# Kernel optimization log

Measured on AMD Instinct MI355X. Metric: run time of the kernel, lower is better.

The kernel has to match this reference:

```python
import jax, jax.numpy as jnp
import numpy as np

LAM = 5.0
NUM_STEPS = 100
B, N, D = 16, 1024, 256


def l2_normalize(x, eps=1e-12):
    # tf.math.l2_normalize: x * rsqrt(max(sum(x^2), eps))
    sq = jnp.sum(x * x, axis=-1, keepdims=True)
    return x * jax.lax.rsqrt(jnp.maximum(sq, eps))


def normalize_pij(P):
    return P / jnp.sum(P, axis=(1, 2), keepdims=True)


def sinkhorn_step(P):
    # a_vec = b_vec = ones(N), so u = 1/col_sum, v = 1/row_sum
    P = P / jnp.sum(P, axis=2, keepdims=True)   # scale rows
    P = P / jnp.sum(P, axis=1, keepdims=True)   # scale cols
    return P


def setup_inputs() -> dict:
    key = jax.random.key(0)
    kA, kB = jax.random.split(key)
    fA = jax.random.normal(kA, (B, N, D), dtype=jnp.float32)
    fB = jax.random.normal(kB, (B, N, D), dtype=jnp.float32)
    return {"fA": fA, "fB": fB}


def reference(fA, fB):
    fA = l2_normalize(fA)
    fB = l2_normalize(fB)
    Sij = jnp.einsum("bnd,bmd->bnm", fA, fB)          # [B, N, N]
    Cij = jnp.clip(-Sij, -15.0 / LAM, 15.0 / LAM)

    # batch_compute_optimal_transport
    P = jnp.exp(-LAM * Cij)
    P = normalize_pij(P)

    def step(P, _):
        return sinkhorn_step(P), None

    P, _ = jax.lax.scan(step, P, None, length=NUM_STEPS)

    # straight-through style re-parameterization
    alpha_beta = jax.lax.stop_gradient(P * jnp.exp(LAM * Cij))
    P0 = alpha_beta * jnp.exp(-LAM * Cij)
    P0 = normalize_pij(P0)
    P_out = sinkhorn_step(P0)
    return (P_out, Sij)
```

## Files before the change

kernel.cpp:

```cpp
#include <hip/hip_runtime.h>
#include <stdint.h>

#define NB 16
#define NN 1024
#define ND 256

typedef __bf16 bf16x8 __attribute__((ext_vector_type(8)));
typedef float f32x4 __attribute__((ext_vector_type(4)));

__device__ __forceinline__ unsigned short f2bf(float x){
  unsigned u = __builtin_bit_cast(unsigned, x);
  u += 0x7FFFu + ((u >> 16) & 1u);
  return (unsigned short)(u >> 16);
}
__device__ __forceinline__ float bflo(unsigned u){ return __builtin_bit_cast(float, u << 16); }
__device__ __forceinline__ float bfhi(unsigned u){ return __builtin_bit_cast(float, u & 0xFFFF0000u); }

__global__ __launch_bounds__(256) void norm_cast_kernel(
    const float* __restrict__ fA, const float* __restrict__ fB,
    unsigned short* __restrict__ Abf, unsigned short* __restrict__ Bbf)
{
  int task = blockIdx.x * 4 + (threadIdx.x >> 6);
  int lane = threadIdx.x & 63;
  const float* src = (task < NB*NN) ? fA : fB;
  unsigned short* dst = (task < NB*NN) ? Abf : Bbf;
  int row = (task < NB*NN) ? task : task - NB*NN;
  float4 x = ((const float4*)(src + (size_t)row*ND))[lane];
  float sq = x.x*x.x + x.y*x.y + x.z*x.z + x.w*x.w;
  #pragma unroll
  for (int off = 32; off > 0; off >>= 1) sq += __shfl_xor(sq, off);
  float s = rsqrtf(fmaxf(sq, 1e-12f));
  ushort4 o;
  o.x = f2bf(x.x*s); o.y = f2bf(x.y*s); o.z = f2bf(x.z*s); o.w = f2bf(x.w*s);
  ((ushort4*)(dst + (size_t)row*ND))[lane] = o;
}

#define LDK 40

__global__ __launch_bounds__(256) void gemm_exp_kernel(
    const unsigned short* __restrict__ Abf, const unsigned short* __restrict__ Bbf,
    float* __restrict__ S, unsigned short* __restrict__ Kg)
{
  __shared__ __align__(16) unsigned short As[128*LDK];
  __shared__ __align__(16) unsigned short Bs[128*LDK];
  const int b = blockIdx.z;
  const int mbase = blockIdx.y * 128;
  const int nbase = blockIdx.x * 128;
  const int t = threadIdx.x;
  const int lane = t & 63;
  const int wave = t >> 6;
  const int wm = wave >> 1, wn = wave & 1;
  const int quad = lane >> 4, l16 = lane & 15;

  const unsigned short* Ab = Abf + (size_t)b*NN*ND;
  const unsigned short* Bb = Bbf + (size_t)b*NN*ND;

  f32x4 acc[4][4];
  #pragma unroll
  for (int i=0;i<4;i++)
    #pragma unroll
    for (int j=0;j<4;j++) acc[i][j] = (f32x4){0.f,0.f,0.f,0.f};

  for (int k0 = 0; k0 < ND; k0 += 32){
    __syncthreads();
    #pragma unroll
    for (int i=0;i<2;i++){
      int chunk = t + 256*i;
      int row = chunk >> 2, seg = chunk & 3;
      *(uint4*)(&As[row*LDK + seg*8]) = *(const uint4*)(Ab + (size_t)(mbase+row)*ND + k0 + seg*8);
      *(uint4*)(&Bs[row*LDK + seg*8]) = *(const uint4*)(Bb + (size_t)(nbase+row)*ND + k0 + seg*8);
    }
    __syncthreads();
    bf16x8 af[4], bg[4];
    #pragma unroll
    for (int i=0;i<4;i++){
      af[i] = *(const bf16x8*)(&As[(wm*64 + i*16 + l16)*LDK + quad*8]);
      bg[i] = *(const bf16x8*)(&Bs[(wn*64 + i*16 + l16)*LDK + quad*8]);
    }
    #pragma unroll
    for (int i=0;i<4;i++)
      #pragma unroll
      for (int j=0;j<4;j++)
        acc[i][j] = __builtin_amdgcn_mfma_f32_16x16x32_bf16(af[i], bg[j], acc[i][j], 0, 0, 0);
  }

  float* Sb = S + (size_t)b*NN*NN;
  unsigned short* Kb = Kg + (size_t)b*NN*NN;
  #pragma unroll
  for (int i=0;i<4;i++){
    #pragma unroll
    for (int j=0;j<4;j++){
      int n = nbase + wn*64 + j*16 + l16;
      #pragma unroll
      for (int v=0;v<4;v++){
        int m = mbase + wm*64 + i*16 + quad*4 + v;
        float sv = acc[i][j][v];
        Sb[(size_t)m*NN + n] = sv;
        float sc = fminf(fmaxf(sv, -3.f), 3.f);
        Kb[(size_t)m*NN + n] = f2bf(__expf(5.f*sc));
      }
    }
  }
}

__global__ __launch_bounds__(1024) void sinkhorn_kernel(
    const unsigned short* __restrict__ Kg, float* __restrict__ P,
    float* __restrict__ slots)
{
  __shared__ __align__(16) float v[NN];
  __shared__ __align__(16) float part[NN];
  __shared__ __align__(16) float u[64];

  const int blk = blockIdx.x;
  const int b  = blk & 15;
  const int rb = blk >> 4;
  const int t = threadIdx.x;
  const int w = t >> 6;
  const int l = t & 63;

  const unsigned short* Kgb = Kg + ((size_t)(b*NN + rb*64))*NN;

  unsigned kcol[32];
  #pragma unroll
  for (int k=0;k<32;k++){
    unsigned lo = Kgb[(size_t)(2*k)*NN + t];
    unsigned hi = Kgb[(size_t)(2*k+1)*NN + t];
    kcol[k] = lo | (hi << 16);
  }
  unsigned krow[32];
  {
    const uint4* rs = (const uint4*)(Kgb + (size_t)l*NN + w*64);
    #pragma unroll
    for (int k=0;k<8;k++){
      uint4 q4 = rs[k];
      krow[4*k+0]=q4.x; krow[4*k+1]=q4.y; krow[4*k+2]=q4.z; krow[4*k+3]=q4.w;
    }
  }
  v[t] = 1.0f;
  __syncthreads();

  const float4* v4 = (const float4*)v;
  const float4* u4 = (const float4*)u;
  float* sl_b = slots + (size_t)b*3*16*NN;
  float* my_slot = sl_b + (size_t)rb*NN + t;

  int buf = 0;
  float vt = 1.0f;
  for (int it = 0; it < 101; it++){
    float rsum = 0.f;
    #pragma unroll
    for (int k=0;k<16;k++){
      float4 vv = v4[w*16 + k];
      unsigned ka = krow[2*k], kb = krow[2*k+1];
      rsum += bflo(ka)*vv.x + bfhi(ka)*vv.y + bflo(kb)*vv.z + bfhi(kb)*vv.w;
    }
    part[w*64 + l] = rsum;
    __syncthreads();
    if (t < 64){
      float s = 0.f;
      #pragma unroll
      for (int q=0;q<16;q++) s += part[q*64 + t];
      u[t] = 1.0f / s;
    }
    __syncthreads();
    float csum = 0.f;
    #pragma unroll
    for (int k=0;k<16;k++){
      float4 uu = u4[k];
      unsigned ka = kcol[2*k], kb = kcol[2*k+1];
      csum += bflo(ka)*uu.x + bfhi(ka)*uu.y + bflo(kb)*uu.z + bfhi(kb)*uu.w;
    }
    __hip_atomic_store(my_slot + (size_t)buf*16*NN, csum,
                       __ATOMIC_RELAXED, __HIP_MEMORY_SCOPE_AGENT);
    const float* base = sl_b + (size_t)buf*16*NN + t;
    float cs;
    for (;;){
      float s0 = 0.f; bool ok = true;
      #pragma unroll
      for (int p=0;p<16;p++){
        float x = __hip_atomic_load(base + (size_t)p*NN,
                                    __ATOMIC_RELAXED, __HIP_MEMORY_SCOPE_AGENT);
        ok &= (x != 0.f);
        s0 += x;
      }
      if (ok){ cs = s0; break; }
      __builtin_amdgcn_s_sleep(1);
    }
    int prev = (buf == 0) ? 2 : buf - 1;
    __hip_atomic_store(my_slot + (size_t)prev*16*NN, 0.f,
                       __ATOMIC_RELAXED, __HIP_MEMORY_SCOPE_AGENT);
    vt = 1.0f / cs;
    v[t] = vt;
    buf = (buf == 2) ? 0 : buf + 1;
    __syncthreads();
  }

  float* Pb = P + ((size_t)(b*NN + rb*64))*NN;
  #pragma unroll
  for (int k=0;k<16;k++){
    float4 uu = u4[k];
    unsigned ka = kcol[2*k], kb = kcol[2*k+1];
    Pb[(size_t)(4*k+0)*NN + t] = bflo(ka)*uu.x*vt;
    Pb[(size_t)(4*k+1)*NN + t] = bfhi(ka)*uu.y*vt;
    Pb[(size_t)(4*k+2)*NN + t] = bflo(kb)*uu.z*vt;
    Pb[(size_t)(4*k+3)*NN + t] = bfhi(kb)*uu.w*vt;
  }
}

extern "C" void kernel_launch(void* const* d_in, const int* in_sizes, int n_in,
                              void* d_out, int out_size, void* d_ws, size_t ws_size,
                              hipStream_t stream)
{
  const float* fA = (const float*)d_in[0];
  const float* fB = (const float*)d_in[1];
  float* Pout = (float*)d_out;
  float* Sout = Pout + (size_t)NB*NN*NN;
  unsigned short* Kg = (unsigned short*)d_out;

  unsigned short* Abf = (unsigned short*)d_ws;
  unsigned short* Bbf = Abf + (size_t)NB*NN*ND;
  float* slots = (float*)((char*)d_ws + (size_t)16*1024*1024);

  hipMemsetAsync(slots, 0, (size_t)NB*3*16*NN*4, stream);
  norm_cast_kernel<<<dim3(8192), dim3(256), 0, stream>>>(fA, fB, Abf, Bbf);
  gemm_exp_kernel<<<dim3(8,8,NB), dim3(256), 0, stream>>>(Abf, Bbf, Sout, Kg);
  sinkhorn_kernel<<<dim3(256), dim3(1024), 0, stream>>>(Kg, Pout, slots);
}
```

Baseline: 1.742 ms.

## Probe for L2-coherent fast path and use workgroup-scope polling in Sinkhorn exchange

Adds a startup handshake in which the 16 blocks of each batch check whether stores and loads at workgroup scope (sc0 only) are seen by the other blocks within a deadline, then agree on a per-batch verdict. If every block passes, the per-iteration cross-block column-sum exchange uses workgroup-scope stores and inline-asm batched sc0 loads instead of agent-scope atomics. The aim is lower latency for the 101 inter-block barrier rounds. The cost is a startup probe, and correctness now depends on the blocks of a batch sharing a coherent L2/XCD, with a fallback to the old path otherwise.

Result: slower. 3.842 ms (+120.6%).

```diff
diff --git a/kernel.cpp b/kernel.cpp
--- a/kernel.cpp
+++ b/kernel.cpp
@@ -103,13 +103,56 @@
   }
 }
 
+__device__ __forceinline__ void store_l2(float* p, float x){
+  __hip_atomic_store(p, x, __ATOMIC_RELAXED, __HIP_MEMORY_SCOPE_WORKGROUP);
+}
+
+__device__ __forceinline__ bool poll8(const float* base, unsigned voff, float thr, float& sum){
+  float x0,x1,x2,x3,x4,x5,x6,x7; unsigned a;
+  asm volatile(
+    "v_mov_b32 %8, %9\n\t"
+    "global_load_dword %0, %8, %10 sc0\n\t"
+    "v_add_u32 %8, 0x1000, %8\n\t"
+    "global_load_dword %1, %8, %10 sc0\n\t"
+    "v_add_u32 %8, 0x1000, %8\n\t"
+    "global_load_dword %2, %8, %10 sc0\n\t"
+    "v_add_u32 %8, 0x1000, %8\n\t"
+    "global_load_dword %3, %8, %10 sc0\n\t"
+    "v_add_u32 %8, 0x1000, %8\n\t"
+    "global_load_dword %4, %8, %10 sc0\n\t"
+    "v_add_u32 %8, 0x1000, %8\n\t"
+    "global_load_dword %5, %8, %10 sc0\n\t"
+    "v_add_u32 %8, 0x1000, %8\n\t"
+    "global_load_dword %6, %8, %10 sc0\n\t"
+    "v_add_u32 %8, 0x1000, %8\n\t"
+    "global_load_dword %7, %8, %10 sc0\n\t"
+    "s_waitcnt vmcnt(0)"
+    : "=&v"(x0),"=&v"(x1),"=&v"(x2),"=&v"(x3),
+      "=&v"(x4),"=&v"(x5),"=&v"(x6),"=&v"(x7),"=&v"(a)
+    : "v"(voff), "s"((uint64_t)(uintptr_t)base)
+    : "memory");
+  bool ok = (x0>thr)&(x1>thr)&(x2>thr)&(x3>thr)&(x4>thr)&(x5>thr)&(x6>thr)&(x7>thr);
+  sum = ((x0+x1)+(x2+x3))+((x4+x5)+(x6+x7));
+  return ok;
+}
+
+__device__ __forceinline__ bool poll16(const float* base, int t, float thr, float& sum){
+  float s0, s1;
+  bool o0 = poll8(base, (unsigned)(t*4), thr, s0);
+  bool o1 = poll8(base, (unsigned)(t*4) + 8u*4096u, thr, s1);
+  sum = s0 + s1;
+  return o0 & o1;
+}
+
 __global__ __launch_bounds__(1024) void sinkhorn_kernel(
     const unsigned short* __restrict__ Kg, float* __restrict__ P,
-    float* __restrict__ slots)
+    float* __restrict__ slots, unsigned* __restrict__ verdict)
 {
   __shared__ __align__(16) float v[NN];
   __shared__ __align__(16) float part[NN];
   __shared__ __align__(16) float u[64];
+  __shared__ int bad;
+  __shared__ int fastflag;
 
   const int blk = blockIdx.x;
   const int b  = blk & 15;
@@ -137,11 +180,57 @@
     }
   }
   v[t] = 1.0f;
-  __syncthreads();
+
+  float* sl_b = slots + (size_t)b*4*16*NN;
+  float* probe_base = sl_b + (size_t)3*16*NN;
+  {
+    float dum;
+    store_l2(probe_base + (size_t)rb*NN + t, 1.0f);
+    bool ok = false;
+    unsigned long long dl = __builtin_amdgcn_s_memrealtime() + 100000ull;
+    for(;;){
+      ok = poll16(probe_base, t, 0.5f, dum);
+      if (ok) break;
+      if (__builtin_amdgcn_s_memrealtime() > dl) break;
+      __builtin_amdgcn_s_sleep(1);
+    }
+    if (ok){
+      store_l2(probe_base + (size_t)rb*NN + t, 2.0f);
+      dl = __builtin_amdgcn_s_memrealtime() + 100000ull;
+      for(;;){
+        if (poll16(probe_base, t, 1.5f, dum)) break;
+        if (__builtin_amdgcn_s_memrealtime() > dl){ ok = false; break; }
+        __builtin_amdgcn_s_sleep(1);
+      }
+    }
+    if (t == 0) bad = 0;
+    __syncthreads();
+    if (!ok) bad = 1;
+    __syncthreads();
+    if (t == 0){
+      unsigned my = bad ? 2u : 1u;
+      __hip_atomic_store(&verdict[b*16 + rb], my,
+                         __ATOMIC_RELAXED, __HIP_MEMORY_SCOPE_AGENT);
+      int f = 1;
+      for(;;){
+        bool pending = false; f = 1;
+        for (int p=0;p<16;p++){
+          unsigned x = __hip_atomic_load(&verdict[b*16 + p],
+                                         __ATOMIC_RELAXED, __HIP_MEMORY_SCOPE_AGENT);
+          if (x == 0u){ pending = true; break; }
+          if (x != 1u) f = 0;
+        }
+        if (!pending) break;
+        __builtin_amdgcn_s_sleep(8);
+      }
+      fastflag = f;
+    }
+    __syncthreads();
+  }
+  const bool fastf = (fastflag != 0);
 
   const float4* v4 = (const float4*)v;
   const float4* u4 = (const float4*)u;
-  float* sl_b = slots + (size_t)b*3*16*NN;
   float* my_slot = sl_b + (size_t)rb*NN + t;
 
   int buf = 0;
@@ -170,25 +259,35 @@
       unsigned ka = kcol[2*k], kb = kcol[2*k+1];
       csum += bflo(ka)*uu.x + bfhi(ka)*uu.y + bflo(kb)*uu.z + bfhi(kb)*uu.w;
     }
-    __hip_atomic_store(my_slot + (size_t)buf*16*NN, csum,
-                       __ATOMIC_RELAXED, __HIP_MEMORY_SCOPE_AGENT);
-    const float* base = sl_b + (size_t)buf*16*NN + t;
     float cs;
-    for (;;){
-      float s0 = 0.f; bool ok = true;
-      #pragma unroll
-      for (int p=0;p<16;p++){
-        float x = __hip_atomic_load(base + (size_t)p*NN,
-                                    __ATOMIC_RELAXED, __HIP_MEMORY_SCOPE_AGENT);
-        ok &= (x != 0.f);
-        s0 += x;
-      }
-      if (ok){ cs = s0; break; }
-      __builtin_amdgcn_s_sleep(1);
-    }
     int prev = (buf == 0) ? 2 : buf - 1;
-    __hip_atomic_store(my_slot + (size_t)prev*16*NN, 0.f,
-                       __ATOMIC_RELAXED, __HIP_MEMORY_SCOPE_AGENT);
+    if (fastf){
+      store_l2(my_slot + (size_t)buf*16*NN, csum);
+      const float* base = sl_b + (size_t)buf*16*NN;
+      for(;;){
+        if (poll16(base, t, 0.0f, cs)) break;
+        __builtin_amdgcn_s_sleep(1);
+      }
+      store_l2(my_slot + (size_t)prev*16*NN, 0.f);
+    } else {
+      __hip_atomic_store(my_slot + (size_t)buf*16*NN, csum,
+                         __ATOMIC_RELAXED, __HIP_MEMORY_SCOPE_AGENT);
+      const float* base = sl_b + (size_t)buf*16*NN + t;
+      for (;;){
+        float s0 = 0.f; bool ok = true;
+        #pragma unroll
+        for (int p=0;p<16;p++){
+          float x = __hip_atomic_load(base + (size_t)p*NN,
+                                      __ATOMIC_RELAXED, __HIP_MEMORY_SCOPE_AGENT);
+          ok &= (x != 0.f);
+          s0 += x;
+        }
+        if (ok){ cs = s0; break; }
+        __builtin_amdgcn_s_sleep(1);
+      }
+      __hip_atomic_store(my_slot + (size_t)prev*16*NN, 0.f,
+                         __ATOMIC_RELAXED, __HIP_MEMORY_SCOPE_AGENT);
+    }
     vt = 1.0f / cs;
     v[t] = vt;
     buf = (buf == 2) ? 0 : buf + 1;
@@ -220,9 +319,10 @@
   unsigned short* Abf = (unsigned short*)d_ws;
   unsigned short* Bbf = Abf + (size_t)NB*NN*ND;
   float* slots = (float*)((char*)d_ws + (size_t)16*1024*1024);
-
-  hipMemsetAsync(slots, 0, (size_t)NB*3*16*NN*4, stream);
+  unsigned* verdict = (unsigned*)(slots + (size_t)NB*4*16*NN);
+
+  hipMemsetAsync(slots, 0, (size_t)NB*4*16*NN*4 + (size_t)NB*16*4, stream);
   norm_cast_kernel<<<dim3(8192), dim3(256), 0, stream>>>(fA, fB, Abf, Bbf);
   gemm_exp_kernel<<<dim3(8,8,NB), dim3(256), 0, stream>>>(Abf, Bbf, Sout, Kg);
-  sinkhorn_kernel<<<dim3(256), dim3(1024), 0, stream>>>(Kg, Pout, slots);
-}
+  sinkhorn_kernel<<<dim3(256), dim3(1024), 0, stream>>>(Kg, Pout, slots, verdict);
+}
```
